# Kernel tuning notes

Hardware: AMD Instinct MI355X
Metric: run time of the kernel (lower is better)

The kernel has to match this reference:

```python
import jax, jax.numpy as jnp
import numpy as np

DIM = 1024
NUM_EXPERTS = 8
TOP_K = 2
B, S = 2, 2048
HID = 4 * DIM


def setup_inputs() -> dict:
    key = jax.random.key(0)
    ks = jax.random.split(key, 7)
    scale = 0.02
    x = jax.random.normal(ks[0], (B, S, DIM), dtype=jnp.float32)
    gate_w = jax.random.normal(ks[1], (DIM, NUM_EXPERTS), dtype=jnp.float32) * scale
    gate_b = jnp.zeros((NUM_EXPERTS,), dtype=jnp.float32)
    w1 = jax.random.normal(ks[2], (NUM_EXPERTS, DIM, HID), dtype=jnp.float32) * scale
    b1 = jnp.zeros((NUM_EXPERTS, HID), dtype=jnp.float32)
    w2 = jax.random.normal(ks[3], (NUM_EXPERTS, HID, DIM), dtype=jnp.float32) * scale
    b2 = jnp.zeros((NUM_EXPERTS, DIM), dtype=jnp.float32)
    return {"x": x, "gate_w": gate_w, "gate_b": gate_b,
            "w1": w1, "b1": b1, "w2": w2, "b2": b2}


def reference(x, gate_w, gate_b, w1, b1, w2, b2):
    # Gate: [B,S,E]
    gates = jnp.einsum('bsd,de->bse', x, gate_w) + gate_b
    top_w, top_idx = jax.lax.top_k(gates, TOP_K)          # [B,S,K]
    probs = jax.nn.softmax(top_w, axis=-1)                # softmax over selected logits
    # Dense all-expert FFN (matches original: every expert runs on every token)
    h = jnp.einsum('bsd,edh->bseh', x, w1) + b1           # [B,S,E,4D]
    h = jax.nn.gelu(h, approximate=False)                 # exact GELU (torch default)
    y = jnp.einsum('bseh,ehd->bsed', h, w2) + b2          # [B,S,E,D]
    # Select top-k experts per token and combine
    sel = jnp.take_along_axis(y, top_idx[..., None], axis=2)   # [B,S,K,D]
    return jnp.sum(sel * probs[..., None], axis=2)        # [B,S,D]
```

## Files before the change

kernel.cpp:

```cpp
#include <hip/hip_runtime.h>
#include <hip/hip_bf16.h>

#define T_TOKENS 4096
#define DIM      1024
#define HID      4096
#define NE       8
#define CAP      4096

typedef __attribute__((ext_vector_type(8))) short  bf16x8;
typedef __attribute__((ext_vector_type(4))) float  f32x4;

__device__ static inline void gll16(const void* g, void* l) {
    __builtin_amdgcn_global_load_lds(
        (const __attribute__((address_space(1))) void*)g,
        (__attribute__((address_space(3))) void*)l,
        16, 0, 0);
}

__global__ __launch_bounds__(64) void gate_kernel(
    const float* __restrict__ x, const float* __restrict__ gw,
    const float* __restrict__ gb, __hip_bfloat16* __restrict__ xb,
    int* __restrict__ counts, int* __restrict__ tlist, float* __restrict__ plist)
{
    const int tok = blockIdx.x;
    const int l   = threadIdx.x;
    const float* xr = x + (size_t)tok * DIM;

    float part[NE];
#pragma unroll
    for (int e = 0; e < NE; e++) part[e] = 0.f;

#pragma unroll
    for (int i = 0; i < DIM / 64; i++) {
        int d = i * 64 + l;
        float xv = xr[d];
        xb[(size_t)tok * DIM + d] = __float2bfloat16(xv);
        const float4* g4 = (const float4*)(gw + (size_t)d * NE);
        float4 a = g4[0], b = g4[1];
        part[0] += xv * a.x; part[1] += xv * a.y;
        part[2] += xv * a.z; part[3] += xv * a.w;
        part[4] += xv * b.x; part[5] += xv * b.y;
        part[6] += xv * b.z; part[7] += xv * b.w;
    }
#pragma unroll
    for (int off = 32; off > 0; off >>= 1) {
#pragma unroll
        for (int e = 0; e < NE; e++) part[e] += __shfl_xor(part[e], off, 64);
    }
    if (l == 0) {
        float lg[NE];
#pragma unroll
        for (int e = 0; e < NE; e++) lg[e] = part[e] + gb[e];
        int i0 = 0;
#pragma unroll
        for (int e = 1; e < NE; e++) if (lg[e] > lg[i0]) i0 = e;
        int i1 = (i0 == 0) ? 1 : 0;
#pragma unroll
        for (int e = 0; e < NE; e++) if (e != i0 && lg[e] > lg[i1]) i1 = e;
        float t  = expf(lg[i1] - lg[i0]);
        float p0 = 1.f / (1.f + t);
        float p1 = t / (1.f + t);
        int pos0 = atomicAdd(&counts[i0], 1);
        tlist[i0 * CAP + pos0] = tok; plist[i0 * CAP + pos0] = p0;
        int pos1 = atomicAdd(&counts[i1], 1);
        tlist[i1 * CAP + pos1] = tok; plist[i1 * CAP + pos1] = p1;
    }
}

__global__ void finalize_kernel(const int* __restrict__ counts, int* __restrict__ base)
{
    if (threadIdx.x == 0) {
        int acc = 0;
        for (int e = 0; e < NE; e++) { base[e] = acc; acc += counts[e]; }
        base[NE] = acc;
    }
}

__global__ __launch_bounds__(256) void transpose_cvt(
    const float* __restrict__ in, __hip_bfloat16* __restrict__ outp, int K, int N)
{
    __shared__ float tile[32][33];
    const int e  = blockIdx.z;
    const float* src = in + (size_t)e * K * N;
    __hip_bfloat16* dst = outp + (size_t)e * K * N;
    const int k0 = blockIdx.y * 32, n0 = blockIdx.x * 32;
    const int tx = threadIdx.x & 31, ty = threadIdx.x >> 5;
#pragma unroll
    for (int i = 0; i < 4; i++)
        tile[ty + i * 8][tx] = src[(size_t)(k0 + ty + i * 8) * N + n0 + tx];
    __syncthreads();
#pragma unroll
    for (int i = 0; i < 4; i++) {
        float v = tile[tx][ty + i * 8];
        dst[(size_t)(n0 + ty + i * 8) * K + k0 + tx] = __float2bfloat16(v);
    }
}

__global__ __launch_bounds__(256, 3) void ffn1_kernel(
    const __hip_bfloat16* __restrict__ xb, const __hip_bfloat16* __restrict__ w1t,
    const float* __restrict__ b1, const int* __restrict__ counts,
    const int* __restrict__ base, const int* __restrict__ tlist,
    __hip_bfloat16* __restrict__ H)
{
    const int e  = blockIdx.z;
    const int ne = counts[e];
    const int rb = blockIdx.y, cb = blockIdx.x;
    if (rb * 128 >= ne) return;

    __shared__ __align__(16) ushort ldsA[2][4096];
    __shared__ __align__(16) ushort ldsB[2][4096];

    const int t = threadIdx.x;
    const int l = t & 63, w = t >> 6;
    const int wr = w >> 1, wc = w & 1;

    const int slot0 = w * 128 + l;
    const int slot1 = w * 128 + 64 + l;
    const int row0 = slot0 >> 2, row1 = slot1 >> 2;
    const int ch0 = ((slot0 & 3) ^ ((row0 >> 1) & 3)) * 8;
    const int ch1 = ((slot1 & 3) ^ ((row1 >> 1) & 3)) * 8;
    const int lo0 = w * 1024;
    const int lo1 = w * 1024 + 512;

    const int r0g = rb * 128 + row0, r1g = rb * 128 + row1;
    const int tok0 = tlist[e * CAP + (r0g < ne ? r0g : 0)];
    const int tok1 = tlist[e * CAP + (r1g < ne ? r1g : 0)];
    const ushort* aS0 = (const ushort*)xb + (size_t)tok0 * DIM + ch0;
    const ushort* aS1 = (const ushort*)xb + (size_t)tok1 * DIM + ch1;
    const ushort* bS0 = (const ushort*)w1t + ((size_t)e * HID + cb * 128 + row0) * DIM + ch0;
    const ushort* bS1 = (const ushort*)w1t + ((size_t)e * HID + cb * 128 + row1) * DIM + ch1;

    f32x4 acc[4][4];
#pragma unroll
    for (int i = 0; i < 4; i++)
#pragma unroll
        for (int j = 0; j < 4; j++) acc[i][j] = (f32x4){0.f, 0.f, 0.f, 0.f};

    const int lm = l & 15, lgp = l >> 4;
    const int rch = (lgp ^ ((lm >> 1) & 3)) * 8;

    gll16(aS0, &ldsA[0][lo0]); gll16(aS1, &ldsA[0][lo1]);
    gll16(bS0, &ldsB[0][lo0]); gll16(bS1, &ldsB[0][lo1]);

    int cur = 0;
    const int NK = DIM / 32;
    for (int ks = 0; ks < NK; ks++) {
        __syncthreads();
        if (ks + 1 < NK) {
            const int ko = (ks + 1) * 32;
            gll16(aS0 + ko, &ldsA[cur ^ 1][lo0]); gll16(aS1 + ko, &ldsA[cur ^ 1][lo1]);
            gll16(bS0 + ko, &ldsB[cur ^ 1][lo0]); gll16(bS1 + ko, &ldsB[cur ^ 1][lo1]);
        }
        bf16x8 af[4], bfr[4];
#pragma unroll
        for (int i = 0; i < 4; i++) {
            int row = wr * 64 + i * 16 + lm;
            af[i] = *(const bf16x8*)&ldsA[cur][row * 32 + rch];
        }
#pragma unroll
        for (int j = 0; j < 4; j++) {
            int row = wc * 64 + j * 16 + lm;
            bfr[j] = *(const bf16x8*)&ldsB[cur][row * 32 + rch];
        }
#pragma unroll
        for (int i = 0; i < 4; i++)
#pragma unroll
            for (int j = 0; j < 4; j++)
                acc[i][j] = __builtin_amdgcn_mfma_f32_16x16x32_bf16(af[i], bfr[j], acc[i][j], 0, 0, 0);
        cur ^= 1;
    }

    const int hb = base[e];
#pragma unroll
    for (int i = 0; i < 4; i++) {
#pragma unroll
        for (int jj = 0; jj < 4; jj++) {
            int r = rb * 128 + wr * 64 + i * 16 + lgp * 4 + jj;
            if (r < ne) {
                size_t hrow = (size_t)(hb + r) * HID;
#pragma unroll
                for (int j = 0; j < 4; j++) {
                    int col = cb * 128 + wc * 64 + j * 16 + lm;
                    float v = acc[i][j][jj] + b1[e * HID + col];
                    v = 0.5f * v * (1.0f + erff(v * 0.70710678118654752f));
                    H[hrow + col] = __float2bfloat16(v);
                }
            }
        }
    }
}

__global__ __launch_bounds__(256, 3) void ffn2_kernel(
    const __hip_bfloat16* __restrict__ H, const __hip_bfloat16* __restrict__ w2t,
    const float* __restrict__ b2, const int* __restrict__ counts,
    const int* __restrict__ base, const int* __restrict__ tlist,
    const float* __restrict__ plist, float* __restrict__ out)
{
    const int e  = blockIdx.z;
    const int ne = counts[e];
    const int rb = blockIdx.y, cb = blockIdx.x;
    if (rb * 128 >= ne) return;

    __shared__ __align__(16) ushort ldsA[2][4096];
    __shared__ __align__(16) ushort ldsB[2][4096];

    const int t = threadIdx.x;
    const int l = t & 63, w = t >> 6;
    const int wr = w >> 1, wc = w & 1;

    const int slot0 = w * 128 + l;
    const int slot1 = w * 128 + 64 + l;
    const int row0 = slot0 >> 2, row1 = slot1 >> 2;
    const int ch0 = ((slot0 & 3) ^ ((row0 >> 1) & 3)) * 8;
    const int ch1 = ((slot1 & 3) ^ ((row1 >> 1) & 3)) * 8;
    const int lo0 = w * 1024;
    const int lo1 = w * 1024 + 512;

    const int hb = base[e];
    const int r0g = rb * 128 + row0, r1g = rb * 128 + row1;
    const int hr0 = hb + (r0g < ne ? r0g : ne - 1);
    const int hr1 = hb + (r1g < ne ? r1g : ne - 1);
    const ushort* aS0 = (const ushort*)H + (size_t)hr0 * HID + ch0;
    const ushort* aS1 = (const ushort*)H + (size_t)hr1 * HID + ch1;
    const ushort* bS0 = (const ushort*)w2t + ((size_t)e * DIM + cb * 128 + row0) * HID + ch0;
    const ushort* bS1 = (const ushort*)w2t + ((size_t)e * DIM + cb * 128 + row1) * HID + ch1;

    f32x4 acc[4][4];
#pragma unroll
    for (int i = 0; i < 4; i++)
#pragma unroll
        for (int j = 0; j < 4; j++) acc[i][j] = (f32x4){0.f, 0.f, 0.f, 0.f};

    const int lm = l & 15, lgp = l >> 4;
    const int rch = (lgp ^ ((lm >> 1) & 3)) * 8;

    gll16(aS0, &ldsA[0][lo0]); gll16(aS1, &ldsA[0][lo1]);
    gll16(bS0, &ldsB[0][lo0]); gll16(bS1, &ldsB[0][lo1]);

    int cur = 0;
    const int NK = HID / 32;
    for (int ks = 0; ks < NK; ks++) {
        __syncthreads();
        if (ks + 1 < NK) {
            const int ko = (ks + 1) * 32;
            gll16(aS0 + ko, &ldsA[cur ^ 1][lo0]); gll16(aS1 + ko, &ldsA[cur ^ 1][lo1]);
            gll16(bS0 + ko, &ldsB[cur ^ 1][lo0]); gll16(bS1 + ko, &ldsB[cur ^ 1][lo1]);
        }
        bf16x8 af[4], bfr[4];
#pragma unroll
        for (int i = 0; i < 4; i++) {
            int row = wr * 64 + i * 16 + lm;
            af[i] = *(const bf16x8*)&ldsA[cur][row * 32 + rch];
        }
#pragma unroll
        for (int j = 0; j < 4; j++) {
            int row = wc * 64 + j * 16 + lm;
            bfr[j] = *(const bf16x8*)&ldsB[cur][row * 32 + rch];
        }
#pragma unroll
        for (int i = 0; i < 4; i++)
#pragma unroll
            for (int j = 0; j < 4; j++)
                acc[i][j] = __builtin_amdgcn_mfma_f32_16x16x32_bf16(af[i], bfr[j], acc[i][j], 0, 0, 0);
        cur ^= 1;
    }

#pragma unroll
    for (int i = 0; i < 4; i++) {
#pragma unroll
        for (int jj = 0; jj < 4; jj++) {
            int r = rb * 128 + wr * 64 + i * 16 + lgp * 4 + jj;
            if (r < ne) {
                int tok  = tlist[e * CAP + r];
                float p  = plist[e * CAP + r];
                float* orow = out + (size_t)tok * DIM;
#pragma unroll
                for (int j = 0; j < 4; j++) {
                    int col = cb * 128 + wc * 64 + j * 16 + lm;
                    float v = (acc[i][j][jj] + b2[e * DIM + col]) * p;
                    unsafeAtomicAdd(&orow[col], v);
                }
            }
        }
    }
}

extern "C" void kernel_launch(void* const* d_in, const int* in_sizes, int n_in,
                              void* d_out, int out_size, void* d_ws, size_t ws_size,
                              hipStream_t stream)
{
    const float* x  = (const float*)d_in[0];
    const float* gw = (const float*)d_in[1];
    const float* gb = (const float*)d_in[2];
    const float* w1 = (const float*)d_in[3];
    const float* b1 = (const float*)d_in[4];
    const float* w2 = (const float*)d_in[5];
    const float* b2 = (const float*)d_in[6];
    float* out = (float*)d_out;

    char* ws = (char*)d_ws;
    __hip_bfloat16* w1t = (__hip_bfloat16*)(ws);
    __hip_bfloat16* w2t = (__hip_bfloat16*)(ws + 67108864);
    __hip_bfloat16* Hb  = (__hip_bfloat16*)(ws + 134217728);
    __hip_bfloat16* xb  = (__hip_bfloat16*)(ws + 201326592);
    int*   tlist  = (int*)  (ws + 209715200);
    float* plist  = (float*)(ws + 209846272);
    int*   counts = (int*)  (ws + 209977344);
    int*   basep  = (int*)  (ws + 209977408);

    hipMemsetAsync(out, 0, (size_t)T_TOKENS * DIM * sizeof(float), stream);
    hipMemsetAsync(counts, 0, 64, stream);

    gate_kernel<<<T_TOKENS, 64, 0, stream>>>(x, gw, gb, xb, counts, tlist, plist);
    finalize_kernel<<<1, 64, 0, stream>>>(counts, basep);

    transpose_cvt<<<dim3(HID / 32, DIM / 32, NE), 256, 0, stream>>>(w1, w1t, DIM, HID);
    transpose_cvt<<<dim3(DIM / 32, HID / 32, NE), 256, 0, stream>>>(w2, w2t, HID, DIM);

    ffn1_kernel<<<dim3(HID / 128, CAP / 128, NE), 256, 0, stream>>>(
        xb, w1t, b1, counts, basep, tlist, Hb);
    ffn2_kernel<<<dim3(DIM / 128, CAP / 128, NE), 256, 0, stream>>>(
        Hb, w2t, b2, counts, basep, tlist, plist, out);
}
```

Measured before the change: 521.2 us.

## Split-K the second expert GEMM and widen weight transpose-convert tiles

The second FFN GEMM now splits the hidden reduction into four slices, each in its own block, and adds partial results into the output with atomics. Only split zero adds the bias. This gives the small per-expert output grid more blocks to fill the GPU, at the cost of four times as many atomic adds. The weight transpose/convert kernel now uses 64x64 tiles with float4 loads and 4-wide bf16 stores to cut memory transactions on the fp32-to-bf16 weight conversion.

```diff
diff --git a/kernel.cpp b/kernel.cpp
--- a/kernel.cpp
+++ b/kernel.cpp
@@ -6,9 +6,17 @@
 #define HID      4096
 #define NE       8
 #define CAP      4096
+#define SPLITS   4
+#define KSP      (HID / SPLITS)
 
 typedef __attribute__((ext_vector_type(8))) short  bf16x8;
 typedef __attribute__((ext_vector_type(4))) float  f32x4;
+typedef __attribute__((ext_vector_type(4))) ushort u16x4;
+
+__device__ static inline ushort f2bf(float f) {
+    __hip_bfloat16 h = __float2bfloat16(f);
+    return *(ushort*)&h;
+}
 
 __device__ static inline void gll16(const void* g, void* l) {
     __builtin_amdgcn_global_load_lds(
@@ -76,23 +84,39 @@
     }
 }
 
-__global__ __launch_bounds__(256) void transpose_cvt(
+__global__ __launch_bounds__(256) void transpose_cvt64(
     const float* __restrict__ in, __hip_bfloat16* __restrict__ outp, int K, int N)
 {
-    __shared__ float tile[32][33];
+    __shared__ ushort tile[64][68];
     const int e  = blockIdx.z;
     const float* src = in + (size_t)e * K * N;
-    __hip_bfloat16* dst = outp + (size_t)e * K * N;
-    const int k0 = blockIdx.y * 32, n0 = blockIdx.x * 32;
-    const int tx = threadIdx.x & 31, ty = threadIdx.x >> 5;
-#pragma unroll
-    for (int i = 0; i < 4; i++)
-        tile[ty + i * 8][tx] = src[(size_t)(k0 + ty + i * 8) * N + n0 + tx];
+    ushort* dst = (ushort*)outp + (size_t)e * K * N;
+    const int k0 = blockIdx.y * 64, n0 = blockIdx.x * 64;
+    const int tid = threadIdx.x;
+
+    const int rn4 = (tid & 15) * 4;
+    const int rk  = tid >> 4;
+#pragma unroll
+    for (int p = 0; p < 4; p++) {
+        int k = rk + p * 16;
+        float4 v = *(const float4*)&src[(size_t)(k0 + k) * N + n0 + rn4];
+        tile[k][rn4 + 0] = f2bf(v.x);
+        tile[k][rn4 + 1] = f2bf(v.y);
+        tile[k][rn4 + 2] = f2bf(v.z);
+        tile[k][rn4 + 3] = f2bf(v.w);
+    }
     __syncthreads();
-#pragma unroll
-    for (int i = 0; i < 4; i++) {
-        float v = tile[tx][ty + i * 8];
-        dst[(size_t)(n0 + ty + i * 8) * K + k0 + tx] = __float2bfloat16(v);
+    const int wk4 = (tid & 15) * 4;
+    const int wn  = tid >> 4;
+#pragma unroll
+    for (int p = 0; p < 4; p++) {
+        int n = wn + p * 16;
+        u16x4 u;
+        u[0] = tile[wk4 + 0][n];
+        u[1] = tile[wk4 + 1][n];
+        u[2] = tile[wk4 + 2][n];
+        u[3] = tile[wk4 + 3][n];
+        *(u16x4*)&dst[(size_t)(n0 + n) * K + k0 + wk4] = u;
     }
 }
 
@@ -198,7 +222,9 @@
 {
     const int e  = blockIdx.z;
     const int ne = counts[e];
-    const int rb = blockIdx.y, cb = blockIdx.x;
+    const int rb = blockIdx.y >> 2;
+    const int sp = blockIdx.y & 3;
+    const int cb = blockIdx.x;
     if (rb * 128 >= ne) return;
 
     __shared__ __align__(16) ushort ldsA[2][4096];
@@ -220,10 +246,11 @@
     const int r0g = rb * 128 + row0, r1g = rb * 128 + row1;
     const int hr0 = hb + (r0g < ne ? r0g : ne - 1);
     const int hr1 = hb + (r1g < ne ? r1g : ne - 1);
-    const ushort* aS0 = (const ushort*)H + (size_t)hr0 * HID + ch0;
-    const ushort* aS1 = (const ushort*)H + (size_t)hr1 * HID + ch1;
-    const ushort* bS0 = (const ushort*)w2t + ((size_t)e * DIM + cb * 128 + row0) * HID + ch0;
-    const ushort* bS1 = (const ushort*)w2t + ((size_t)e * DIM + cb * 128 + row1) * HID + ch1;
+    const size_t ko0 = (size_t)sp * KSP;
+    const ushort* aS0 = (const ushort*)H + (size_t)hr0 * HID + ko0 + ch0;
+    const ushort* aS1 = (const ushort*)H + (size_t)hr1 * HID + ko0 + ch1;
+    const ushort* bS0 = (const ushort*)w2t + ((size_t)e * DIM + cb * 128 + row0) * HID + ko0 + ch0;
+    const ushort* bS1 = (const ushort*)w2t + ((size_t)e * DIM + cb * 128 + row1) * HID + ko0 + ch1;
 
     f32x4 acc[4][4];
 #pragma unroll
@@ -238,7 +265,7 @@
     gll16(bS0, &ldsB[0][lo0]); gll16(bS1, &ldsB[0][lo1]);
 
     int cur = 0;
-    const int NK = HID / 32;
+    const int NK = KSP / 32;
     for (int ks = 0; ks < NK; ks++) {
         __syncthreads();
         if (ks + 1 < NK) {
@@ -277,8 +304,9 @@
 #pragma unroll
                 for (int j = 0; j < 4; j++) {
                     int col = cb * 128 + wc * 64 + j * 16 + lm;
-                    float v = (acc[i][j][jj] + b2[e * DIM + col]) * p;
-                    unsafeAtomicAdd(&orow[col], v);
+                    float v = acc[i][j][jj];
+                    if (sp == 0) v += b2[e * DIM + col];
+                    unsafeAtomicAdd(&orow[col], v * p);
                 }
             }
         }
@@ -314,11 +342,11 @@
     gate_kernel<<<T_TOKENS, 64, 0, stream>>>(x, gw, gb, xb, counts, tlist, plist);
     finalize_kernel<<<1, 64, 0, stream>>>(counts, basep);
 
-    transpose_cvt<<<dim3(HID / 32, DIM / 32, NE), 256, 0, stream>>>(w1, w1t, DIM, HID);
-    transpose_cvt<<<dim3(DIM / 32, HID / 32, NE), 256, 0, stream>>>(w2, w2t, HID, DIM);
+    transpose_cvt64<<<dim3(HID / 64, DIM / 64, NE), 256, 0, stream>>>(w1, w1t, DIM, HID);
+    transpose_cvt64<<<dim3(DIM / 64, HID / 64, NE), 256, 0, stream>>>(w2, w2t, HID, DIM);
 
     ffn1_kernel<<<dim3(HID / 128, CAP / 128, NE), 256, 0, stream>>>(
         xb, w1t, b1, counts, basep, tlist, Hb);
-    ffn2_kernel<<<dim3(DIM / 128, CAP / 128, NE), 256, 0, stream>>>(
+    ffn2_kernel<<<dim3(DIM / 128, (CAP / 128) * SPLITS, NE), 256, 0, stream>>>(
         Hb, w2t, b2, counts, basep, tlist, plist, out);
 }
```

New measurement: 540.8 us. +3.8%, slower.
